# Performance work log

Measured on AMD Instinct MI355X. Metric: run time of the kernel, lower is better.

The kernel has to match this reference:

```python
import jax, jax.numpy as jnp
import numpy as np

BATCH, LENGTH, HIDDEN, SSM = 32, 2048, 128, 256


def setup_inputs() -> dict:
    key = jax.random.key(0)
    ks = jax.random.split(key, 7)
    b_std = 1.0 / np.sqrt(HIDDEN)
    c_std = 1.0 / np.sqrt(SSM)
    return {
        "inputs": jax.random.normal(ks[0], (BATCH, LENGTH, HIDDEN), jnp.float32),
        "A_diag": jax.random.normal(ks[1], (SSM,), jnp.float32),
        "G_diag": jax.random.uniform(ks[2], (SSM,), jnp.float32),
        "steps": jax.random.normal(ks[3], (SSM,), jnp.float32) * 0.5,
        "B": jax.random.uniform(ks[4], (SSM, HIDDEN, 2), jnp.float32, -b_std, b_std),
        "C": jax.random.uniform(ks[5], (HIDDEN, SSM, 2), jnp.float32, -c_std, c_std),
        "D": jax.random.normal(ks[6], (HIDDEN,), jnp.float32),
    }


def _project_parameters(A_diag, G_diag, steps):
    # Mirrors DampedLinOSSLayer._project_parameters: sigmoid step, relu damping,
    # and clamp A into the band where the 2x2 IMEX1 transition has complex eigenvalues.
    step = jax.nn.sigmoid(steps)
    g = jax.nn.relu(G_diag)
    denom = jnp.maximum(step * step, 1e-6)
    s = step * g
    base = jnp.sqrt(jnp.maximum(1.0 + s, 1e-6))
    a_low = (2.0 + s - 2.0 * base) / denom
    a_high = (2.0 + s + 2.0 * base) / denom
    a = a_low + jax.nn.relu(A_diag - a_low) - jax.nn.relu(A_diag - a_high)
    return a, g, step


def _eigenvalue(a, g, step):
    # IMEX1 transition M = [[S, -S*dt*A], [dt*S, 1 - dt^2*S*A]] with S = 1/(1+dt*G).
    # det(M) = S, trace(M) = S + 1 - dt^2*S*A; projection guarantees trace^2 < 4*det,
    # so eigenvalues form a conjugate pair lam = T/2 + i*sqrt(S - T^2/4).
    S = 1.0 / (1.0 + step * g)
    T = S + 1.0 - step * step * S * a
    imag = jnp.sqrt(jnp.maximum(S - 0.25 * T * T, 0.0))
    return jax.lax.complex(0.5 * T, imag)  # [P] complex64


def reference(inputs, A_diag, G_diag, steps, B, C, D):
    a, g, step = _project_parameters(A_diag, G_diag, steps)
    lam = _eigenvalue(a, g, step)  # [P]

    # Complex input projection: bu = (B_re + i*B_im) @ u, shape [batch, L, P]
    bu = jax.lax.complex(
        jnp.einsum("blh,ph->blp", inputs, B[..., 0]),
        jnp.einsum("blh,ph->blp", inputs, B[..., 1]),
    )

    # Diagonal complex linear recurrence x_k = lam * x_{k-1} + bu_k via associative scan.
    def combine(e1, e2):
        a1, b1 = e1
        a2, b2 = e2
        return a1 * a2, a2 * b1 + b2

    lam_b = jnp.broadcast_to(lam[None, None, :], bu.shape)
    _, states = jax.lax.associative_scan(combine, (lam_b, bu), axis=1)

    # Output: Re(C @ x) + D * u
    projected = (
        jnp.einsum("blp,hp->blh", states.real, C[..., 0])
        - jnp.einsum("blp,hp->blh", states.imag, C[..., 1])
    )
    return projected + inputs * D
```

## Files before the change

### kernel.cpp

```cpp
#include <hip/hip_runtime.h>
#include <hip/hip_bf16.h>
#include <math.h>

#define BATCH 32
#define LEN   2048
#define HID   128
#define SSM   256

#define BPL 32768

typedef __attribute__((ext_vector_type(4))) float f32x4;
typedef __attribute__((ext_vector_type(8))) short bf16x8;
typedef __attribute__((ext_vector_type(4))) int   i32x4;

static __device__ __forceinline__ unsigned short f2bf(float x) {
    union { float f; unsigned u; } v; v.f = x;
    unsigned r = (v.u + 0x7FFFu + ((v.u >> 16) & 1u)) >> 16;
    return (unsigned short)r;
}
static __device__ __forceinline__ unsigned short f2bf_hi(float x) {
    union { float f; unsigned u; } v; v.f = x;
    return (unsigned short)(v.u >> 16);
}
static __device__ __forceinline__ float bf2f(unsigned short b) {
    union { unsigned u; float f; } v; v.u = ((unsigned)b) << 16;
    return v.f;
}
static __device__ __forceinline__ unsigned int cvtpk(float a, float b) {
    __hip_bfloat162 h = __float22bfloat162_rn(float2{a, b});
    union { __hip_bfloat162 h2; unsigned int u; } c; c.h2 = h;
    return c.u;
}
static __device__ __forceinline__ void cmul(float& rr, float& ri,
                                            float ar, float ai, float br, float bi) {
    rr = ar * br - ai * bi;
    ri = ar * bi + ai * br;
}
static __device__ __forceinline__ void gload16(const void* g, void* l) {
    __builtin_amdgcn_global_load_lds(
        (const __attribute__((address_space(1))) unsigned int*)g,
        (__attribute__((address_space(3))) unsigned int*)l,
        16, 0, 0);
}

__global__ __launch_bounds__(256) void k0b_prep(const float* __restrict__ Bm,
                                                const float* __restrict__ Cm,
                                                const float* __restrict__ A,
                                                const float* __restrict__ G,
                                                const float* __restrict__ steps,
                                                unsigned short* __restrict__ Bsp,
                                                unsigned short* __restrict__ C2,
                                                float* __restrict__ lam) {
    if (blockIdx.x == 256) {
        int p = threadIdx.x;
        if (p < SSM) {
            float stp   = 1.f / (1.f + expf(-steps[p]));
            float g     = fmaxf(G[p], 0.f);
            float denom = fmaxf(stp * stp, 1e-6f);
            float s     = stp * g;
            float base  = sqrtf(fmaxf(1.f + s, 1e-6f));
            float alow  = (2.f + s - 2.f * base) / denom;
            float ahigh = (2.f + s + 2.f * base) / denom;
            float a     = alow + fmaxf(A[p] - alow, 0.f) - fmaxf(A[p] - ahigh, 0.f);
            float S     = 1.f / (1.f + stp * g);
            float T     = S + 1.f - stp * stp * S * a;
            lam[p]       = 0.5f * T;
            lam[SSM + p] = sqrtf(fmaxf(S - 0.25f * T * T, 0.f));
        }
        return;
    }
    int gidx = blockIdx.x * 256 + threadIdx.x;
    if (gidx < 32768) {
        int p = gidx >> 7, h = gidx & 127;
        float vr = Bm[(size_t)(p * HID + h) * 2];
        float vi = Bm[(size_t)(p * HID + h) * 2 + 1];
        unsigned short hh = f2bf_hi(vr);
        Bsp[0 * BPL + p * HID + h] = hh;
        Bsp[1 * BPL + p * HID + h] = f2bf(vr - bf2f(hh));
        hh = f2bf_hi(vi);
        Bsp[2 * BPL + p * HID + h] = hh;
        Bsp[3 * BPL + p * HID + h] = f2bf(vi - bf2f(hh));
    } else {
        int g2 = gidx - 32768;
        int h = g2 >> 8, p = g2 & 255;
        float vr = Cm[(size_t)(h * SSM + p) * 2];
        float vi = -Cm[(size_t)(h * SSM + p) * 2 + 1];
        unsigned short rh = f2bf_hi(vr);
        unsigned short ih = f2bf_hi(vi);
        size_t rowh = (size_t)h * 512;
        C2[rowh + 2 * p]               = rh;
        C2[rowh + 2 * p + 1]           = ih;
        C2[65536 + rowh + 2 * p]       = f2bf(vr - bf2f(rh));
        C2[65536 + rowh + 2 * p + 1]   = f2bf(vi - bf2f(ih));
    }
}

__global__ __launch_bounds__(256) void ku_cvt(const float* __restrict__ u,
                                              unsigned short* __restrict__ ubf) {
    const int total = BATCH * LEN * HID;
    const int stride = 2048 * 256 * 8;
    for (int i = (blockIdx.x * 256 + threadIdx.x) * 8; i < total; i += stride) {
        f32x4 a = *(const f32x4*)&u[i];
        f32x4 c = *(const f32x4*)&u[i + 4];
        i32x4 o;
        o[0] = (int)cvtpk(a[0], a[1]);
        o[1] = (int)cvtpk(a[2], a[3]);
        o[2] = (int)cvtpk(c[0], c[1]);
        o[3] = (int)cvtpk(c[2], c[3]);
        *(i32x4*)&ubf[i] = o;
    }
}

__global__ __launch_bounds__(512, 4) void k12_fused(const unsigned short* __restrict__ ubf,
                                                    const unsigned short* __restrict__ Bsp,
                                                    const float* __restrict__ lam,
                                                    unsigned short* __restrict__ TP) {
    __shared__ __align__(16) char sU[2][32768];
    __shared__ __align__(16) char sT2[10240];
    __shared__ float Rld[4][2][8][2];

    int d    = blockIdx.x;
    int xcd  = d & 7;
    int idx  = d >> 3;
    int pt   = idx & 15;
    int bhi  = idx >> 4;
    int b    = bhi * 8 + xcd;
    int p0   = pt * 16;

    int tid  = threadIdx.x;
    int lane = tid & 63, w = tid >> 6;
    int wl   = w >> 1, wp = w & 1;
    int fr   = lane & 15, g = lane >> 4;
    int frp  = fr & 7;
    int comp = fr >> 3;
    int pcol = p0 + wp * 8 + frp;

    const unsigned short* Bh  = Bsp + (size_t)(comp * 2) * BPL + (size_t)pcol * HID;
    const unsigned short* Blo = Bsp + (size_t)(comp * 2 + 1) * BPL + (size_t)pcol * HID;
    bf16x8 Bfh[4], Bfl[4];
#pragma unroll
    for (int kc = 0; kc < 4; ++kc) {
        Bfh[kc] = *(const bf16x8*)&Bh[kc * 32 + g * 8];
        Bfl[kc] = *(const bf16x8*)&Blo[kc * 32 + g * 8];
    }

    float pw_r[4], pw_i[4];
    float lg_r, lg_i;
    float l4r, l4i, l8r, l8i, l16r, l16i, l32r, l32i;
    {
        float ar = lam[pcol], ai = lam[SSM + pcol];
        pw_r[0] = ar; pw_i[0] = ai;
        cmul(pw_r[1], pw_i[1], ar, ai, ar, ai);
        cmul(pw_r[2], pw_i[2], pw_r[1], pw_i[1], ar, ai);
        cmul(pw_r[3], pw_i[3], pw_r[1], pw_i[1], pw_r[1], pw_i[1]);
        l4r = pw_r[3]; l4i = pw_i[3];
        cmul(l8r, l8i, l4r, l4i, l4r, l4i);
        cmul(l16r, l16i, l8r, l8i, l8r, l8i);
        cmul(l32r, l32i, l16r, l16i, l16r, l16i);
        if (g == 0)      { lg_r = 1.f; lg_i = 0.f; }
        else if (g == 1) { lg_r = l4r; lg_i = l4i; }
        else if (g == 2) { lg_r = l8r; lg_i = l8i; }
        else             { cmul(lg_r, lg_i, l8r, l8i, l4r, l4i); }
    }

    float TCr = 0.f, TCi = 0.f;

    const unsigned short* ub = ubf + (size_t)b * (LEN * HID);
    int srow32  = tid >> 4;
    int stg_src = srow32 * HID + ((((tid & 15) * 16) ^ ((srow32 & 7) << 4)) >> 1);

#define STAGE(buf, tt)                                                        \
    {                                                                         \
        const unsigned short* gs = ub + (size_t)(tt) * 16384 + stg_src;       \
        char* ls = &sU[buf][tid * 16];                                        \
        _Pragma("unroll")                                                     \
        for (int q = 0; q < 4; ++q)                                           \
            gload16(gs + q * 4096, ls + q * 8192);                            \
    }

    STAGE(0, 0)
    __syncthreads();
    int cur = 0;

    for (int t = 0; t < 16; ++t) {
        int l0t = t * 128;

        if (t < 15) STAGE(cur ^ 1, t + 1)

        const char* su = &sU[cur][0];
        f32x4 acc[2];
        acc[0] = (f32x4)(0.f); acc[1] = (f32x4)(0.f);
#pragma unroll
        for (int kc = 0; kc < 4; ++kc) {
#pragma unroll
            for (int mi = 0; mi < 2; ++mi) {
                int off = (wl * 32 + mi * 16 + fr) * 256 + ((kc * 64 + g * 16) ^ ((fr & 7) << 4));
                bf16x8 ah = *(const bf16x8*)(su + off);
                acc[mi] = __builtin_amdgcn_mfma_f32_16x16x32_bf16(ah, Bfh[kc], acc[mi], 0, 0, 0);
                acc[mi] = __builtin_amdgcn_mfma_f32_16x16x32_bf16(ah, Bfl[kc], acc[mi], 0, 0, 0);
            }
        }

        float xr[4], xi[4];
#pragma unroll
        for (int e = 0; e < 4; ++e) {
            float send = (comp == 0) ? acc[1][e] : acc[0][e];
            float oth  = __shfl_xor(send, 8, 64);
            xr[e] = (comp == 0) ? acc[0][e] : oth;
            xi[e] = (comp == 0) ? oth       : acc[1][e];
        }

        float Er, Ei, Fr, Fi, For, Foi;
        {
            float lr = pw_r[0], li = pw_i[0];
            float cr = 0.f, ci = 0.f;
#pragma unroll
            for (int r = 0; r < 4; ++r) {
                float nr = fmaf(lr, cr, fmaf(-li, ci, xr[r]));
                float ni = fmaf(lr, ci, fmaf(li, cr, xi[r]));
                cr = nr; ci = ni;
                xr[r] = cr; xi[r] = ci;
            }
            float Qr = cr, Qi = ci;
            float ur = __shfl_up(Qr, 16u, 64);
            float ui = __shfl_up(Qi, 16u, 64);
            if (g >= 1) {
                Qr = fmaf(l4r, ur, fmaf(-l4i, ui, Qr));
                Qi = fmaf(l4r, ui, fmaf(l4i, ur, Qi));
            }
            ur = __shfl_up(Qr, 32u, 64);
            ui = __shfl_up(Qi, 32u, 64);
            if (g >= 2) {
                Qr = fmaf(l8r, ur, fmaf(-l8i, ui, Qr));
                Qi = fmaf(l8r, ui, fmaf(l8i, ur, Qi));
            }
            Er = __shfl_up(Qr, 16u, 64);
            Ei = __shfl_up(Qi, 16u, 64);
            if (g == 0) { Er = 0.f; Ei = 0.f; }
            Fr = __shfl(Qr, fr + 48, 64);
            Fi = __shfl(Qi, fr + 48, 64);
            For = __shfl_xor(Fr, 8, 64);
            Foi = __shfl_xor(Fi, 8, 64);
            float Rr = fmaf(l16r, For, fmaf(-l16i, Foi, Fr));
            float Ri = fmaf(l16r, Foi, fmaf(l16i, For, Fi));
            if (g == 0 && fr >= 8) { Rld[wl][wp][frp][0] = Rr; Rld[wl][wp][frp][1] = Ri; }
        }
        __syncthreads();

        {
            float Wr = TCr, Wi = TCi;
            float Tr = TCr, Ti = TCi;
#pragma unroll
            for (int w2 = 0; w2 < 4; ++w2) {
                float rr = Rld[w2][wp][frp][0], ri = Rld[w2][wp][frp][1];
                float nTr = fmaf(l32r, Tr, fmaf(-l32i, Ti, rr));
                float nTi = fmaf(l32r, Ti, fmaf(l32i, Tr, ri));
                Tr = nTr; Ti = nTi;
                if (w2 < wl) {
                    float nWr = fmaf(l32r, Wr, fmaf(-l32i, Wi, rr));
                    float nWi = fmaf(l32r, Wi, fmaf(l32i, Wr, ri));
                    Wr = nWr; Wi = nWi;
                }
            }
            TCr = Tr; TCi = Ti;
            float prr, pri;
            if (comp == 0) { prr = Wr; pri = Wi; }
            else {
                prr = fmaf(l16r, Wr, fmaf(-l16i, Wi, For));
                pri = fmaf(l16r, Wi, fmaf(l16i, Wr, Foi));
            }
            float Mr = fmaf(lg_r, prr, fmaf(-lg_i, pri, Er));
            float Mi = fmaf(lg_r, pri, fmaf(lg_i, prr, Ei));
#pragma unroll
            for (int r = 0; r < 4; ++r) {
                xr[r] = fmaf(pw_r[r], Mr, fmaf(-pw_i[r], Mi, xr[r]));
                xi[r] = fmaf(pw_r[r], Mi, fmaf(pw_i[r], Mr, xi[r]));
            }
        }

        {
            int colb  = wl * 32 + comp * 16 + g * 4;
            int idxu  = wp * 8 + frp;
            int piece = idxu >> 2, sub = idxu & 3;
            int pw    = piece ^ g;
#pragma unroll
            for (int r = 0; r < 4; ++r) {
                unsigned int pk = cvtpk(xr[r], xi[r]);
                *(unsigned int*)(sT2 + (colb + r) * 80 + pw * 16 + sub * 4) = pk;
            }
        }
        __syncthreads();

        {
            int row = tid >> 2, q = tid & 3;
            int x2  = (row >> 2) & 3;
            bf16x8 v = *(const bf16x8*)(sT2 + row * 80 + ((q ^ x2) * 16));
            *(bf16x8*)&TP[((size_t)(b * LEN) + l0t + row) * 512 + p0 * 2 + q * 8] = v;
        }
        cur ^= 1;
    }
#undef STAGE
}

__global__ __launch_bounds__(256, 4) void k3_out(const unsigned short* __restrict__ TP,
                                                 const unsigned short* __restrict__ C2,
                                                 const unsigned short* __restrict__ ubf,
                                                 const float* __restrict__ D,
                                                 float* __restrict__ out) {
    __shared__ __align__(16) char sAB[2][16384];

    int d    = blockIdx.x;
    int xcd  = d & 7;
    int rest = d >> 3;
    int ht   = rest & 1;
    int lt   = (rest >> 1) & 15;
    int bhi  = rest >> 5;
    int b    = bhi * 8 + xcd;
    int l0   = lt * 128;
    int h0   = ht * 64;

    int tid = threadIdx.x;
    int lane = tid & 63, w = tid >> 6;
    int wl = w >> 1, wh = w & 1;
    int fr = lane & 15, g = lane >> 4;

    f32x4 acc[4][2];
#pragma unroll
    for (int mi = 0; mi < 4; ++mi)
#pragma unroll
        for (int ni = 0; ni < 2; ++ni) acc[mi][ni] = (f32x4)(0.f);

    float dv[2];
#pragma unroll
    for (int ni = 0; ni < 2; ++ni) dv[ni] = D[h0 + wh * 32 + ni * 16 + fr];

#define STAGE3(buf, cc)                                                       \
    {                                                                         \
        _Pragma("unroll")                                                     \
        for (int q = 0; q < 2; ++q) {                                         \
            int dg = tid + q * 256; int rw = dg >> 2, sl = dg & 3;            \
            gload16(TP + ((size_t)(b * LEN) + l0 + rw) * 512 + (cc) * 32 +    \
                        ((sl ^ (rw & 3)) * 8),                                \
                    &sAB[buf][dg * 16]);                                      \
        }                                                                     \
        _Pragma("unroll")                                                     \
        for (int q = 0; q < 2; ++q) {                                         \
            int dg = tid + q * 256; int hl = dg >> 8, hr = (dg >> 2) & 63;    \
            int sl = dg & 3;                                                  \
            gload16(C2 + ((size_t)(hl * 128 + h0 + hr)) * 512 + (cc) * 32 +   \
                        ((sl ^ (hr & 3)) * 8),                                \
                    &sAB[buf][8192 + dg * 16]);                               \
        }                                                                     \
    }

    STAGE3(0, 0)
    __syncthreads();
    int cur = 0;

    for (int c = 0; c < 16; ++c) {
        if (c < 15) STAGE3(cur ^ 1, c + 1)

        const char* sb = &sAB[cur][0];
        int swz = (g ^ (fr & 3)) * 16;
        bf16x8 bfr[2][2];
#pragma unroll
        for (int ni = 0; ni < 2; ++ni) {
            int hrow = wh * 32 + ni * 16 + fr;
#pragma unroll
            for (int hl = 0; hl < 2; ++hl)
                bfr[ni][hl] = *(const bf16x8*)(sb + 8192 + hl * 4096 + hrow * 64 + swz);
        }
#pragma unroll
        for (int mi = 0; mi < 4; ++mi) {
            int arow = wl * 64 + mi * 16 + fr;
            bf16x8 af = *(const bf16x8*)(sb + arow * 64 + swz);
#pragma unroll
            for (int ni = 0; ni < 2; ++ni) {
                acc[mi][ni] = __builtin_amdgcn_mfma_f32_16x16x32_bf16(af, bfr[ni][0], acc[mi][ni], 0, 0, 0);
                acc[mi][ni] = __builtin_amdgcn_mfma_f32_16x16x32_bf16(af, bfr[ni][1], acc[mi][ni], 0, 0, 0);
            }
        }
        __syncthreads();
        cur ^= 1;
    }
#undef STAGE3

#pragma unroll
    for (int mi = 0; mi < 4; ++mi)
#pragma unroll
        for (int ni = 0; ni < 2; ++ni) {
            int lb = l0 + wl * 64 + mi * 16 + g * 4;
            int h  = h0 + wh * 32 + ni * 16 + fr;
#pragma unroll
            for (int r = 0; r < 4; ++r) {
                size_t idx = ((size_t)b * LEN + lb + r) * HID + h;
                out[idx] = acc[mi][ni][r] + bf2f(ubf[idx]) * dv[ni];
            }
        }
}

extern "C" void kernel_launch(void* const* d_in, const int* in_sizes, int n_in,
                              void* d_out, int out_size, void* d_ws, size_t ws_size,
                              hipStream_t stream) {
    const float* u  = (const float*)d_in[0];
    const float* A  = (const float*)d_in[1];
    const float* G  = (const float*)d_in[2];
    const float* st = (const float*)d_in[3];
    const float* B  = (const float*)d_in[4];
    const float* C  = (const float*)d_in[5];
    const float* D  = (const float*)d_in[6];
    float* out = (float*)d_out;

    char* WS = (char*)d_ws;
    unsigned short* TP  = (unsigned short*)WS;
    float* lam          = (float*)(WS + 67108864);
    unsigned short* Bsp = (unsigned short*)(WS + 67110912);
    unsigned short* C2  = (unsigned short*)(WS + 67373056);
    unsigned short* ubf = (unsigned short*)(WS + 67635200);

    k0b_prep<<<257, 256, 0, stream>>>(B, C, A, G, st, Bsp, C2, lam);
    ku_cvt<<<2048, 256, 0, stream>>>(u, ubf);
    k12_fused<<<512, 512, 0, stream>>>(ubf, Bsp, lam, TP);
    k3_out<<<1024, 256, 0, stream>>>(TP, C2, ubf, D, out);
}
```

Baseline: 90.84 us.

## Widen output GEMM tile to full hidden dimension with 512-thread blocks

```diff
diff --git a/kernel.cpp b/kernel.cpp
--- a/kernel.cpp
+++ b/kernel.cpp
@@ -302,52 +302,51 @@
 #undef STAGE
 }
 
-__global__ __launch_bounds__(256, 4) void k3_out(const unsigned short* __restrict__ TP,
+__global__ __launch_bounds__(512, 4) void k3_out(const unsigned short* __restrict__ TP,
                                                  const unsigned short* __restrict__ C2,
                                                  const unsigned short* __restrict__ ubf,
                                                  const float* __restrict__ D,
                                                  float* __restrict__ out) {
-    __shared__ __align__(16) char sAB[2][16384];
+    __shared__ __align__(16) char sAB[2][24576];
 
     int d    = blockIdx.x;
     int xcd  = d & 7;
     int rest = d >> 3;
-    int ht   = rest & 1;
-    int lt   = (rest >> 1) & 15;
-    int bhi  = rest >> 5;
+    int lt   = rest & 15;
+    int bhi  = rest >> 4;
     int b    = bhi * 8 + xcd;
     int l0   = lt * 128;
-    int h0   = ht * 64;
 
     int tid = threadIdx.x;
     int lane = tid & 63, w = tid >> 6;
     int wl = w >> 1, wh = w & 1;
     int fr = lane & 15, g = lane >> 4;
 
-    f32x4 acc[4][2];
-#pragma unroll
-    for (int mi = 0; mi < 4; ++mi)
-#pragma unroll
-        for (int ni = 0; ni < 2; ++ni) acc[mi][ni] = (f32x4)(0.f);
-
-    float dv[2];
-#pragma unroll
-    for (int ni = 0; ni < 2; ++ni) dv[ni] = D[h0 + wh * 32 + ni * 16 + fr];
+    f32x4 acc[2][4];
+#pragma unroll
+    for (int mi = 0; mi < 2; ++mi)
+#pragma unroll
+        for (int ni = 0; ni < 4; ++ni) acc[mi][ni] = (f32x4)(0.f);
+
+    float dv[4];
+#pragma unroll
+    for (int ni = 0; ni < 4; ++ni) dv[ni] = D[wh * 64 + ni * 16 + fr];
 
 #define STAGE3(buf, cc)                                                       \
     {                                                                         \
+                                                  \
+        {                                                                     \
+            int rw = tid >> 2, sl = tid & 3;                                  \
+            gload16(TP + ((size_t)(b * LEN) + l0 + rw) * 512 + (cc) * 32 +    \
+                        ((sl ^ (rw & 3)) * 8),                                \
+                    &sAB[buf][tid * 16]);                                     \
+        }                                                                     \
+                                             \
         _Pragma("unroll")                                                     \
         for (int q = 0; q < 2; ++q) {                                         \
-            int dg = tid + q * 256; int rw = dg >> 2, sl = dg & 3;            \
-            gload16(TP + ((size_t)(b * LEN) + l0 + rw) * 512 + (cc) * 32 +    \
-                        ((sl ^ (rw & 3)) * 8),                                \
-                    &sAB[buf][dg * 16]);                                      \
-        }                                                                     \
-        _Pragma("unroll")                                                     \
-        for (int q = 0; q < 2; ++q) {                                         \
-            int dg = tid + q * 256; int hl = dg >> 8, hr = (dg >> 2) & 63;    \
-            int sl = dg & 3;                                                  \
-            gload16(C2 + ((size_t)(hl * 128 + h0 + hr)) * 512 + (cc) * 32 +   \
+            int dg = tid + q * 512;                                           \
+            int hl = dg >> 9, hr = (dg >> 2) & 127, sl = dg & 3;              \
+            gload16(C2 + ((size_t)(hl * 128 + hr)) * 512 + (cc) * 32 +        \
                         ((sl ^ (hr & 3)) * 8),                                \
                     &sAB[buf][8192 + dg * 16]);                               \
         }                                                                     \
@@ -362,22 +361,21 @@
 
         const char* sb = &sAB[cur][0];
         int swz = (g ^ (fr & 3)) * 16;
-        bf16x8 bfr[2][2];
-#pragma unroll
-        for (int ni = 0; ni < 2; ++ni) {
-            int hrow = wh * 32 + ni * 16 + fr;
-#pragma unroll
-            for (int hl = 0; hl < 2; ++hl)
-                bfr[ni][hl] = *(const bf16x8*)(sb + 8192 + hl * 4096 + hrow * 64 + swz);
-        }
-#pragma unroll
-        for (int mi = 0; mi < 4; ++mi) {
-            int arow = wl * 64 + mi * 16 + fr;
-            bf16x8 af = *(const bf16x8*)(sb + arow * 64 + swz);
-#pragma unroll
-            for (int ni = 0; ni < 2; ++ni) {
-                acc[mi][ni] = __builtin_amdgcn_mfma_f32_16x16x32_bf16(af, bfr[ni][0], acc[mi][ni], 0, 0, 0);
-                acc[mi][ni] = __builtin_amdgcn_mfma_f32_16x16x32_bf16(af, bfr[ni][1], acc[mi][ni], 0, 0, 0);
+        bf16x8 af[2];
+#pragma unroll
+        for (int mi = 0; mi < 2; ++mi) {
+            int arow = wl * 32 + mi * 16 + fr;
+            af[mi] = *(const bf16x8*)(sb + arow * 64 + swz);
+        }
+#pragma unroll
+        for (int ni = 0; ni < 4; ++ni) {
+            int hrow = wh * 64 + ni * 16 + fr;
+            bf16x8 ch = *(const bf16x8*)(sb + 8192 + hrow * 64 + swz);
+            bf16x8 cl = *(const bf16x8*)(sb + 8192 + 8192 + hrow * 64 + swz);
+#pragma unroll
+            for (int mi = 0; mi < 2; ++mi) {
+                acc[mi][ni] = __builtin_amdgcn_mfma_f32_16x16x32_bf16(af[mi], ch, acc[mi][ni], 0, 0, 0);
+                acc[mi][ni] = __builtin_amdgcn_mfma_f32_16x16x32_bf16(af[mi], cl, acc[mi][ni], 0, 0, 0);
             }
         }
         __syncthreads();
@@ -386,11 +384,11 @@
 #undef STAGE3
 
 #pragma unroll
-    for (int mi = 0; mi < 4; ++mi)
-#pragma unroll
-        for (int ni = 0; ni < 2; ++ni) {
-            int lb = l0 + wl * 64 + mi * 16 + g * 4;
-            int h  = h0 + wh * 32 + ni * 16 + fr;
+    for (int mi = 0; mi < 2; ++mi)
+#pragma unroll
+        for (int ni = 0; ni < 4; ++ni) {
+            int lb = l0 + wl * 32 + mi * 16 + g * 4;
+            int h  = wh * 64 + ni * 16 + fr;
 #pragma unroll
             for (int r = 0; r < 4; ++r) {
                 size_t idx = ((size_t)b * LEN + lb + r) * HID + h;
@@ -421,5 +419,5 @@
     k0b_prep<<<257, 256, 0, stream>>>(B, C, A, G, st, Bsp, C2, lam);
     ku_cvt<<<2048, 256, 0, stream>>>(u, ubf);
     k12_fused<<<512, 512, 0, stream>>>(ubf, Bsp, lam, TP);
-    k3_out<<<1024, 256, 0, stream>>>(TP, C2, ubf, D, out);
-}
+    k3_out<<<512, 512, 0, stream>>>(TP, C2, ubf, D, out);
+}
```

Result: faster. 86.44 us (-4.8%).
